# Kernel optimization log

Hardware: AMD Instinct MI355X
Metric: run time of the kernel (lower is better)

## Reference

```python
import jax, jax.numpy as jnp
import numpy as np

B, N = 1, 320  # embed_dim == seq_len == N is forced by the module's bmm shapes


def setup_inputs() -> dict:
    key = jax.random.key(0)
    k1, k2, k3, k4 = jax.random.split(key, 4)
    s = jax.random.normal(k1, (B, N, N), dtype=jnp.float32)
    futrue = jax.random.normal(k2, (B, N, N, N), dtype=jnp.float32)
    # nn.Linear(embed_dim, embed_dim) params
    lim = 1.0 / np.sqrt(N)
    W = jax.random.uniform(k3, (N, N), minval=-lim, maxval=lim, dtype=jnp.float32)
    b = jax.random.uniform(k4, (N,), minval=-lim, maxval=lim, dtype=jnp.float32)
    return {"s": s, "futrue": futrue, "W": W, "b": b}


def reference(s, futrue, W, b):
    # futrue = self.fc(futrue): Linear on last dim  [B,T,T,E]
    futP = jnp.einsum('bitj,ej->bite', futrue, W) + b
    # fc = s.transpose(1,2) @ futrue : [B,1,E,T] @ [B,T,T,E] -> [B,T,E,E]
    scores = jnp.einsum('bte,bitj->biej', s, futP)
    fc = jax.nn.softmax(scores, axis=-1)          # softmax over last dim
    # vectorized loop: t_i = fc[:, i].sum(1).unsqueeze(-2).bmm(s)
    w = fc.sum(axis=2)                            # [B, T, T] (sum over e)
    out = jnp.einsum('bij,bjk->bik', w, s)        # concat of all t_i -> [B, T, E]
    return out
```

## Files before the change

kernel.cpp:

```cpp
#include <hip/hip_runtime.h>
#include <hip/hip_bf16.h>
#include <math.h>

#define N 320
#define NN (N * N)

typedef float f32x16 __attribute__((ext_vector_type(16)));
typedef short s16x8  __attribute__((ext_vector_type(8)));

#define MFMA32(a, b, c) __builtin_amdgcn_mfma_f32_32x32x16_bf16((a), (b), (c), 0, 0, 0)

union U4V { uint4 q; s16x8 v; };
union UAV { unsigned u[4]; s16x8 v; };

__device__ inline void split2(float x0, float x1, unsigned& hi, unsigned& lo) {
    unsigned u0 = __float_as_uint(x0), u1 = __float_as_uint(x1);
    hi = (u0 >> 16) | (u1 & 0xFFFF0000u);
    float d0 = x0 - __uint_as_float(u0 & 0xFFFF0000u);
    float d1 = x1 - __uint_as_float(u1 & 0xFFFF0000u);
    lo = (__float_as_uint(d0) >> 16) | (__float_as_uint(d1) & 0xFFFF0000u);
}

__global__ __launch_bounds__(256) void prep_kernel(
    const float* __restrict__ s, const float* __restrict__ W,
    float* __restrict__ wbuf, float* __restrict__ out, float* __restrict__ colsum,
    uint4* __restrict__ spH, uint4* __restrict__ spL,
    uint4* __restrict__ wpH, uint4* __restrict__ wpL)
{
    const int bid = blockIdx.x;
    const int tid = threadIdx.x;
    if (bid < 100) {
        ((float4*)wbuf)[bid * 256 + tid] = make_float4(0.f, 0.f, 0.f, 0.f);
    } else if (bid < 200) {
        ((float4*)out)[(bid - 100) * 256 + tid] = make_float4(0.f, 0.f, 0.f, 0.f);
    } else if (bid < 202) {
        int e = (bid - 200) * 256 + tid;
        if (e < N) {
            const float* sp = s + e;
            float a[8];
#pragma unroll
            for (int u = 0; u < 8; ++u) a[u] = 0.f;
            for (int t = 0; t < N; t += 8) {
#pragma unroll
                for (int u = 0; u < 8; ++u) a[u] += sp[(size_t)(t + u) * N];
            }
            colsum[e] = ((a[0] + a[1]) + (a[2] + a[3])) + ((a[4] + a[5]) + (a[6] + a[7]));
        }
    } else if (bid < 252) {
        int sub = (bid - 202) * 4 + (tid >> 6);
        int l = tid & 63;
        int et = sub / 20, ts = sub % 20;
        int e = et * 32 + (l & 31);
        int t0 = ts * 16 + (l >> 5) * 8;
        unsigned hi[4], lo[4];
#pragma unroll
        for (int d = 0; d < 4; ++d)
            split2(s[(size_t)(t0 + 2 * d) * N + e], s[(size_t)(t0 + 2 * d + 1) * N + e],
                   hi[d], lo[d]);
        spH[sub * 64 + l] = make_uint4(hi[0], hi[1], hi[2], hi[3]);
        spL[sub * 64 + l] = make_uint4(lo[0], lo[1], lo[2], lo[3]);
    } else {
        int sub = (bid - 252) * 4 + (tid >> 6);
        int l = tid & 63;
        int jt = sub / 20, ks = sub % 20;
        int j = jt * 32 + (l & 31);
        int k0 = ks * 16 + (l >> 5) * 8;
        const float* wr = W + (size_t)j * N + k0;
        unsigned hi[4], lo[4];
#pragma unroll
        for (int d = 0; d < 4; ++d) split2(wr[2 * d], wr[2 * d + 1], hi[d], lo[d]);
        wpH[sub * 64 + l] = make_uint4(hi[0], hi[1], hi[2], hi[3]);
        wpL[sub * 64 + l] = make_uint4(lo[0], lo[1], lo[2], lo[3]);
    }
}

__global__ __launch_bounds__(640, 4) void fused64_kernel(
    const float* __restrict__ fut,
    const uint4* __restrict__ spH, const uint4* __restrict__ spL,
    const uint4* __restrict__ wpH, const uint4* __restrict__ wpL,
    const float* __restrict__ bvec, const float* __restrict__ colsum,
    float* __restrict__ w)
{
    extern __shared__ char smraw[];
    unsigned short* Gsh = (unsigned short*)smraw;
    float* Ssh = (float*)smraw;

    const int bid = blockIdx.x;
    const int x  = bid & 7;
    const int g  = bid >> 3;
    const int iw = g / 5, eq = g % 5;
    const int i  = iw * 8 + x;
    const int tid = threadIdx.x;
    const int wid = tid >> 6;
    const int lane = tid & 63;
    const int l31 = lane & 31;
    const int hf  = lane >> 5;

    f32x16 acc0, acc1;
#pragma unroll
    for (int r = 0; r < 16; ++r) { acc0[r] = 0.f; acc1[r] = 0.f; }

    const float* fbase = fut + (size_t)i * NN + (size_t)(hf * 8) * N + wid * 32 + l31;
    const uint4* aH0 = spH + (size_t)((eq * 2 + 0) * 20) * 64 + lane;
    const uint4* aL0 = spL + (size_t)((eq * 2 + 0) * 20) * 64 + lane;
    const uint4* aH1 = spH + (size_t)((eq * 2 + 1) * 20) * 64 + lane;
    const uint4* aL1 = spL + (size_t)((eq * 2 + 1) * 20) * 64 + lane;

#pragma unroll 2
    for (int ts = 0; ts < 20; ++ts) {
        const float* fp = fbase + (size_t)(ts * 16) * N;
        float f[8];
#pragma unroll
        for (int m = 0; m < 8; ++m) f[m] = fp[(size_t)m * N];
        UAV bh, bl;
#pragma unroll
        for (int d = 0; d < 4; ++d) split2(f[2 * d], f[2 * d + 1], bh.u[d], bl.u[d]);
        U4V a0h, a0l, a1h, a1l;
        a0h.q = aH0[ts * 64]; a0l.q = aL0[ts * 64];
        a1h.q = aH1[ts * 64]; a1l.q = aL1[ts * 64];
        acc0 = MFMA32(a0h.v, bh.v, acc0);
        acc1 = MFMA32(a1h.v, bh.v, acc1);
        acc0 = MFMA32(a0l.v, bh.v, acc0);
        acc1 = MFMA32(a1l.v, bh.v, acc1);
        acc0 = MFMA32(a0h.v, bl.v, acc0);
        acc1 = MFMA32(a1h.v, bl.v, acc1);
    }

    {
        unsigned short* GH0 = Gsh;
        unsigned short* GL0 = Gsh + 10240;
        unsigned short* GH1 = Gsh + 20480;
        unsigned short* GL1 = Gsh + 30720;
        const int c  = wid * 4 + (l31 >> 3);
        const int jj = l31 & 7;
        const int sw = c & 7;
#pragma unroll
        for (int r = 0; r < 16; ++r) {
            int e = (r & 3) + ((r >> 2) << 3) + (hf << 2);
            int off = (c * 32 + (e ^ sw)) * 8 + jj;
            {
                float xv = acc0[r];
                unsigned u = __float_as_uint(xv);
                float d = xv - __uint_as_float(u & 0xFFFF0000u);
                GH0[off] = (unsigned short)(u >> 16);
                GL0[off] = (unsigned short)(__float_as_uint(d) >> 16);
            }
            {
                float xv = acc1[r];
                unsigned u = __float_as_uint(xv);
                float d = xv - __uint_as_float(u & 0xFFFF0000u);
                GH1[off] = (unsigned short)(u >> 16);
                GL1[off] = (unsigned short)(__float_as_uint(d) >> 16);
            }
        }
    }
    __syncthreads();

    f32x16 p0a, p0b, p1a, p1b;
#pragma unroll
    for (int r = 0; r < 16; ++r) { p0a[r] = 0.f; p0b[r] = 0.f; p1a[r] = 0.f; p1b[r] = 0.f; }

    const uint4* bHp = wpH + (size_t)(wid * 20) * 64 + lane;
    const uint4* bLp = wpL + (size_t)(wid * 20) * 64 + lane;
    const unsigned short* GH0 = Gsh;
    const unsigned short* GL0 = Gsh + 10240;
    const unsigned short* GH1 = Gsh + 20480;
    const unsigned short* GL1 = Gsh + 30720;

#pragma unroll 2
    for (int ks = 0; ks < 20; ++ks) {
        int c = ks * 2 + hf;
        int off = (c * 32 + (l31 ^ (c & 7))) * 8;
        s16x8 gh0 = *(const s16x8*)&GH0[off];
        s16x8 gl0 = *(const s16x8*)&GL0[off];
        s16x8 gh1 = *(const s16x8*)&GH1[off];
        s16x8 gl1 = *(const s16x8*)&GL1[off];
        U4V wh, wl;
        wh.q = bHp[ks * 64];
        wl.q = bLp[ks * 64];
        p0a = MFMA32(gh0, wh.v, p0a);
        p1a = MFMA32(gh1, wh.v, p1a);
        p0b = MFMA32(gl0, wh.v, p0b);
        p1b = MFMA32(gl1, wh.v, p1b);
        p0b = MFMA32(gh0, wl.v, p0b);
        p1b = MFMA32(gh1, wl.v, p1b);
    }

    const int jcol = wid * 32 + l31;
    const float bj = bvec[jcol];
    float v0[16], v1[16];
#pragma unroll
    for (int r = 0; r < 16; ++r) {
        int e = (r & 3) + ((r >> 2) << 3) + (hf << 2);
        v0[r] = (p0a[r] + p0b[r]) + colsum[eq * 64 + e] * bj;
        v1[r] = (p1a[r] + p1b[r]) + colsum[eq * 64 + 32 + e] * bj;
    }
    __syncthreads();

#pragma unroll
    for (int r = 0; r < 16; ++r) {
        int e = (r & 3) + ((r >> 2) << 3) + (hf << 2);
        Ssh[e * 320 + jcol] = v0[r];
        Ssh[(32 + e) * 320 + jcol] = v1[r];
    }
    __syncthreads();

    const int hw = tid >> 5;
    const int li = tid & 31;
#pragma unroll
    for (int q = 0; q < 4; ++q) {
        int row = q * 20 + hw;
        if (row < 64) {
            float xr[10];
            float m = -3.4e38f;
#pragma unroll
            for (int k = 0; k < 10; ++k) {
                xr[k] = Ssh[row * 320 + li + 32 * k];
                m = fmaxf(m, xr[k]);
            }
#pragma unroll
            for (int off = 16; off; off >>= 1) m = fmaxf(m, __shfl_xor(m, off, 64));
            float ss = 0.f;
#pragma unroll
            for (int k = 0; k < 10; ++k) ss += __expf(xr[k] - m);
#pragma unroll
            for (int off = 16; off; off >>= 1) ss += __shfl_xor(ss, off, 64);
            if (li == 0) { Ssh[row * 320 + 0] = m; Ssh[row * 320 + 1] = 1.0f / ss; }
        }
    }
    __syncthreads();

    float wcol = 0.f;
#pragma unroll
    for (int r = 0; r < 16; ++r) {
        int e = (r & 3) + ((r >> 2) << 3) + (hf << 2);
        wcol += __expf(v0[r] - Ssh[e * 320]) * Ssh[e * 320 + 1];
        wcol += __expf(v1[r] - Ssh[(32 + e) * 320]) * Ssh[(32 + e) * 320 + 1];
    }
    wcol += __shfl_xor(wcol, 32, 64);
    if (hf == 0) atomicAdd(&w[(size_t)i * N + jcol], wcol);
}

__global__ __launch_bounds__(320) void out_gemm_kernel(
    const float* __restrict__ w, const float* __restrict__ s,
    float* __restrict__ out)
{
    const int i = blockIdx.x;
    const int jc = blockIdx.y;
    const int k = threadIdx.x;
    const float* wr = w + (size_t)i * N + jc * 80;
    const float* sp = s + (size_t)(jc * 80) * N + k;
    float a0 = 0.f, a1 = 0.f, a2 = 0.f, a3 = 0.f;
    for (int j = 0; j < 80; j += 4) {
        a0 += wr[j + 0] * sp[(size_t)(j + 0) * N];
        a1 += wr[j + 1] * sp[(size_t)(j + 1) * N];
        a2 += wr[j + 2] * sp[(size_t)(j + 2) * N];
        a3 += wr[j + 3] * sp[(size_t)(j + 3) * N];
    }
    atomicAdd(&out[(size_t)i * N + k], (a0 + a1) + (a2 + a3));
}

extern "C" void kernel_launch(void* const* d_in, const int* in_sizes, int n_in,
                              void* d_out, int out_size, void* d_ws, size_t ws_size,
                              hipStream_t stream)
{
    const float* s    = (const float*)d_in[0];
    const float* fut  = (const float*)d_in[1];
    const float* W    = (const float*)d_in[2];
    const float* bvec = (const float*)d_in[3];
    float* out = (float*)d_out;

    char* base = (char*)d_ws;
    float* wbuf   = (float*)base;
    float* colsum = (float*)(base + 409600);
    uint4* spH = (uint4*)(base + 410880);
    uint4* spL = (uint4*)(base + 615680);
    uint4* wpH = (uint4*)(base + 820480);
    uint4* wpL = (uint4*)(base + 1025280);

    static bool attr_done = false;
    if (!attr_done) {
        (void)hipFuncSetAttribute((const void*)fused64_kernel,
                                  hipFuncAttributeMaxDynamicSharedMemorySize, 81920);
        attr_done = true;
    }

    prep_kernel<<<dim3(302), dim3(256), 0, stream>>>(
        s, W, wbuf, out, colsum, spH, spL, wpH, wpL);

    fused64_kernel<<<dim3(1600), dim3(640), 81920, stream>>>(
        fut, spH, spL, wpH, wpL, bvec, colsum, wbuf);

    out_gemm_kernel<<<dim3(N, 4), dim3(320), 0, stream>>>(wbuf, s, out);
}
```

Measured before the change: 369.3 us.

## Stage fut tiles via async LDS loads, split accumulators, fuse output GEMM

The fused kernel now double-buffers each 16-row slice of fut into shared memory using global_load_lds instead of strided per-lane global loads. The hi and lo correction MFMAs go into separate accumulators so their dependency chains can overlap. The separate out_gemm kernel is removed: a per-row done counter lets the last of the five blocks for row i compute out[i] = w[i]·s directly, which drops one launch and the zeroing of out. The cost is extra __syncthreads in the main loop, an atomic counter with a threadfence, and a serial 320-long dot product done by a single block per row.

```diff
diff --git a/kernel.cpp b/kernel.cpp
--- a/kernel.cpp
+++ b/kernel.cpp
@@ -7,6 +7,7 @@
 
 typedef float f32x16 __attribute__((ext_vector_type(16)));
 typedef short s16x8  __attribute__((ext_vector_type(8)));
+typedef unsigned int u32;
 
 #define MFMA32(a, b, c) __builtin_amdgcn_mfma_f32_32x32x16_bf16((a), (b), (c), 0, 0, 0)
 
@@ -23,7 +24,7 @@
 
 __global__ __launch_bounds__(256) void prep_kernel(
     const float* __restrict__ s, const float* __restrict__ W,
-    float* __restrict__ wbuf, float* __restrict__ out, float* __restrict__ colsum,
+    float* __restrict__ wbuf, float* __restrict__ colsum, unsigned* __restrict__ done,
     uint4* __restrict__ spH, uint4* __restrict__ spL,
     uint4* __restrict__ wpH, uint4* __restrict__ wpL)
 {
@@ -31,11 +32,10 @@
     const int tid = threadIdx.x;
     if (bid < 100) {
         ((float4*)wbuf)[bid * 256 + tid] = make_float4(0.f, 0.f, 0.f, 0.f);
-    } else if (bid < 200) {
-        ((float4*)out)[(bid - 100) * 256 + tid] = make_float4(0.f, 0.f, 0.f, 0.f);
-    } else if (bid < 202) {
-        int e = (bid - 200) * 256 + tid;
+    } else if (bid < 102) {
+        int e = (bid - 100) * 256 + tid;
         if (e < N) {
+            done[e] = 0u;
             const float* sp = s + e;
             float a[8];
 #pragma unroll
@@ -46,8 +46,8 @@
             }
             colsum[e] = ((a[0] + a[1]) + (a[2] + a[3])) + ((a[4] + a[5]) + (a[6] + a[7]));
         }
-    } else if (bid < 252) {
-        int sub = (bid - 202) * 4 + (tid >> 6);
+    } else if (bid < 152) {
+        int sub = (bid - 102) * 4 + (tid >> 6);
         int l = tid & 63;
         int et = sub / 20, ts = sub % 20;
         int e = et * 32 + (l & 31);
@@ -60,7 +60,7 @@
         spH[sub * 64 + l] = make_uint4(hi[0], hi[1], hi[2], hi[3]);
         spL[sub * 64 + l] = make_uint4(lo[0], lo[1], lo[2], lo[3]);
     } else {
-        int sub = (bid - 252) * 4 + (tid >> 6);
+        int sub = (bid - 152) * 4 + (tid >> 6);
         int l = tid & 63;
         int jt = sub / 20, ks = sub % 20;
         int j = jt * 32 + (l & 31);
@@ -75,15 +75,16 @@
 }
 
 __global__ __launch_bounds__(640, 4) void fused64_kernel(
-    const float* __restrict__ fut,
+    const float* __restrict__ fut, const float* __restrict__ s,
     const uint4* __restrict__ spH, const uint4* __restrict__ spL,
     const uint4* __restrict__ wpH, const uint4* __restrict__ wpL,
     const float* __restrict__ bvec, const float* __restrict__ colsum,
-    float* __restrict__ w)
+    float* __restrict__ w, float* __restrict__ out, unsigned* __restrict__ done)
 {
     extern __shared__ char smraw[];
     unsigned short* Gsh = (unsigned short*)smraw;
     float* Ssh = (float*)smraw;
+    __shared__ unsigned lastflag;
 
     const int bid = blockIdx.x;
     const int x  = bid & 7;
@@ -96,34 +97,53 @@
     const int l31 = lane & 31;
     const int hf  = lane >> 5;
 
-    f32x16 acc0, acc1;
-#pragma unroll
-    for (int r = 0; r < 16; ++r) { acc0[r] = 0.f; acc1[r] = 0.f; }
-
-    const float* fbase = fut + (size_t)i * NN + (size_t)(hf * 8) * N + wid * 32 + l31;
+    float* fb0 = (float*)smraw;
+    float* fb1 = (float*)(smraw + 20480);
+
+    auto stageF = [&](int ts, float* buf) {
+        const float* src = fut + (size_t)i * NN + (size_t)ts * (16 * N);
+#pragma unroll
+        for (int r = 0; r < 2; ++r) {
+            const float* gp = src + r * 2560 + wid * 256 + lane * 4;
+            float* lp = buf + r * 2560 + wid * 256;
+            __builtin_amdgcn_global_load_lds(
+                (const u32 __attribute__((address_space(1)))*)gp,
+                (u32 __attribute__((address_space(3)))*)lp, 16, 0, 0);
+        }
+    };
+
+    f32x16 c0, c1, c2, c3;
+#pragma unroll
+    for (int r = 0; r < 16; ++r) { c0[r] = 0.f; c1[r] = 0.f; c2[r] = 0.f; c3[r] = 0.f; }
+
     const uint4* aH0 = spH + (size_t)((eq * 2 + 0) * 20) * 64 + lane;
     const uint4* aL0 = spL + (size_t)((eq * 2 + 0) * 20) * 64 + lane;
     const uint4* aH1 = spH + (size_t)((eq * 2 + 1) * 20) * 64 + lane;
     const uint4* aL1 = spL + (size_t)((eq * 2 + 1) * 20) * 64 + lane;
 
-#pragma unroll 2
+    stageF(0, fb0);
+    __syncthreads();
+    stageF(1, fb1);
+
     for (int ts = 0; ts < 20; ++ts) {
-        const float* fp = fbase + (size_t)(ts * 16) * N;
+        const float* cb = (ts & 1) ? fb1 : fb0;
         float f[8];
 #pragma unroll
-        for (int m = 0; m < 8; ++m) f[m] = fp[(size_t)m * N];
+        for (int m = 0; m < 8; ++m) f[m] = cb[(hf * 8 + m) * 320 + wid * 32 + l31];
         UAV bh, bl;
 #pragma unroll
         for (int d = 0; d < 4; ++d) split2(f[2 * d], f[2 * d + 1], bh.u[d], bl.u[d]);
         U4V a0h, a0l, a1h, a1l;
         a0h.q = aH0[ts * 64]; a0l.q = aL0[ts * 64];
         a1h.q = aH1[ts * 64]; a1l.q = aL1[ts * 64];
-        acc0 = MFMA32(a0h.v, bh.v, acc0);
-        acc1 = MFMA32(a1h.v, bh.v, acc1);
-        acc0 = MFMA32(a0l.v, bh.v, acc0);
-        acc1 = MFMA32(a1l.v, bh.v, acc1);
-        acc0 = MFMA32(a0h.v, bl.v, acc0);
-        acc1 = MFMA32(a1h.v, bl.v, acc1);
+        c0 = MFMA32(a0h.v, bh.v, c0);
+        c1 = MFMA32(a1h.v, bh.v, c1);
+        c2 = MFMA32(a0l.v, bh.v, c2);
+        c3 = MFMA32(a1l.v, bh.v, c3);
+        c2 = MFMA32(a0h.v, bl.v, c2);
+        c3 = MFMA32(a1h.v, bl.v, c3);
+        __syncthreads();
+        if (ts + 2 < 20) stageF(ts + 2, (ts & 1) ? fb1 : fb0);
     }
 
     {
@@ -139,14 +159,14 @@
             int e = (r & 3) + ((r >> 2) << 3) + (hf << 2);
             int off = (c * 32 + (e ^ sw)) * 8 + jj;
             {
-                float xv = acc0[r];
+                float xv = c0[r] + c2[r];
                 unsigned u = __float_as_uint(xv);
                 float d = xv - __uint_as_float(u & 0xFFFF0000u);
                 GH0[off] = (unsigned short)(u >> 16);
                 GL0[off] = (unsigned short)(__float_as_uint(d) >> 16);
             }
             {
-                float xv = acc1[r];
+                float xv = c1[r] + c3[r];
                 unsigned u = __float_as_uint(xv);
                 float d = xv - __uint_as_float(u & 0xFFFF0000u);
                 GH1[off] = (unsigned short)(u >> 16);
@@ -239,25 +259,28 @@
     }
     wcol += __shfl_xor(wcol, 32, 64);
     if (hf == 0) atomicAdd(&w[(size_t)i * N + jcol], wcol);
-}
-
-__global__ __launch_bounds__(320) void out_gemm_kernel(
-    const float* __restrict__ w, const float* __restrict__ s,
-    float* __restrict__ out)
-{
-    const int i = blockIdx.x;
-    const int jc = blockIdx.y;
-    const int k = threadIdx.x;
-    const float* wr = w + (size_t)i * N + jc * 80;
-    const float* sp = s + (size_t)(jc * 80) * N + k;
-    float a0 = 0.f, a1 = 0.f, a2 = 0.f, a3 = 0.f;
-    for (int j = 0; j < 80; j += 4) {
-        a0 += wr[j + 0] * sp[(size_t)(j + 0) * N];
-        a1 += wr[j + 1] * sp[(size_t)(j + 1) * N];
-        a2 += wr[j + 2] * sp[(size_t)(j + 2) * N];
-        a3 += wr[j + 3] * sp[(size_t)(j + 3) * N];
-    }
-    atomicAdd(&out[(size_t)i * N + k], (a0 + a1) + (a2 + a3));
+
+    __threadfence();
+    __syncthreads();
+    if (tid == 0) lastflag = (atomicAdd(&done[i], 1u) == 4u) ? 1u : 0u;
+    __syncthreads();
+    if (lastflag) {
+        float* wrow = Ssh;
+        if (tid < N) wrow[tid] = atomicAdd(&w[(size_t)i * N + tid], 0.0f);
+        __syncthreads();
+        if (tid < N) {
+            const int k = tid;
+            const float* sp = s + k;
+            float a0 = 0.f, a1 = 0.f, a2 = 0.f, a3 = 0.f;
+            for (int j = 0; j < N; j += 4) {
+                a0 += wrow[j + 0] * sp[(size_t)(j + 0) * N];
+                a1 += wrow[j + 1] * sp[(size_t)(j + 1) * N];
+                a2 += wrow[j + 2] * sp[(size_t)(j + 2) * N];
+                a3 += wrow[j + 3] * sp[(size_t)(j + 3) * N];
+            }
+            out[(size_t)i * N + k] = (a0 + a1) + (a2 + a3);
+        }
+    }
 }
 
 extern "C" void kernel_launch(void* const* d_in, const int* in_sizes, int n_in,
@@ -271,12 +294,13 @@
     float* out = (float*)d_out;
 
     char* base = (char*)d_ws;
-    float* wbuf   = (float*)base;
-    float* colsum = (float*)(base + 409600);
-    uint4* spH = (uint4*)(base + 410880);
-    uint4* spL = (uint4*)(base + 615680);
-    uint4* wpH = (uint4*)(base + 820480);
-    uint4* wpL = (uint4*)(base + 1025280);
+    float* wbuf     = (float*)base;
+    float* colsum   = (float*)(base + 409600);
+    unsigned* done  = (unsigned*)(base + 410880);
+    uint4* spH = (uint4*)(base + 412160);
+    uint4* spL = (uint4*)(base + 616960);
+    uint4* wpH = (uint4*)(base + 821760);
+    uint4* wpL = (uint4*)(base + 1026560);
 
     static bool attr_done = false;
     if (!attr_done) {
@@ -285,11 +309,9 @@
         attr_done = true;
     }
 
-    prep_kernel<<<dim3(302), dim3(256), 0, stream>>>(
-        s, W, wbuf, out, colsum, spH, spL, wpH, wpL);
+    prep_kernel<<<dim3(202), dim3(256), 0, stream>>>(
+        s, W, wbuf, colsum, done, spH, spL, wpH, wpL);
 
     fused64_kernel<<<dim3(1600), dim3(640), 81920, stream>>>(
-        fut, spH, spL, wpH, wpL, bvec, colsum, wbuf);
-
-    out_gemm_kernel<<<dim3(N, 4), dim3(320), 0, stream>>>(wbuf, s, out);
+        fut, s, spH, spL, wpH, wpL, bvec, colsum, wbuf, out, done);
 }
```

Result: slower. 748.8 us (+102.8%).
